# Optimization experiments

Hardware: AMD Instinct MI355X
Metric: run time of the kernel (lower is better)

Reference implementation:

```python
import jax, jax.numpy as jnp
import numpy as np

N_NODES = 50000
N_EDGES = 600000
IN_CH = 128
HID = 128
OUT_CH = 1
N_GRAPHS = 64


def setup_inputs() -> dict:
    key = jax.random.key(0)
    ks = jax.random.split(key, 16)
    inp = {
        "x": jax.random.normal(ks[0], (N_NODES, IN_CH), dtype=jnp.float32),
        "edge_index": jax.random.randint(ks[1], (2, N_EDGES), 0, N_NODES, dtype=jnp.int64),
        "edge_weight": jax.random.uniform(ks[2], (N_EDGES,), dtype=jnp.float32),
        "batch": jnp.sort(jax.random.randint(ks[3], (N_NODES,), 0, N_GRAPHS, dtype=jnp.int64)),
    }
    # SAGEConv params: lin_l (neighbor-aggregate path, has bias) and lin_r (root path)
    dims = [(IN_CH, HID), (HID, HID), (HID, HID), (HID, HID)]
    for i, (din, dout) in enumerate(dims, start=1):
        s = 1.0 / np.sqrt(din)
        inp[f"Wl{i}"] = jax.random.uniform(ks[3 + 2 * i], (din, dout), minval=-s, maxval=s, dtype=jnp.float32)
        inp[f"Wr{i}"] = jax.random.uniform(ks[4 + 2 * i], (din, dout), minval=-s, maxval=s, dtype=jnp.float32)
        inp[f"b{i}"] = jnp.zeros((dout,), dtype=jnp.float32)
    s = 1.0 / np.sqrt(HID)
    inp["Wc"] = jax.random.uniform(ks[14], (HID, OUT_CH), minval=-s, maxval=s, dtype=jnp.float32)
    inp["bc"] = jnp.zeros((OUT_CH,), dtype=jnp.float32)
    return inp


def _sage_conv(x, src, dst, Wl, Wr, b):
    # mean aggregation of source-node features at each destination node
    msg = x[src]  # [E, d] gather
    agg = jax.ops.segment_sum(msg, dst, num_segments=N_NODES)
    cnt = jax.ops.segment_sum(jnp.ones((src.shape[0],), x.dtype), dst, num_segments=N_NODES)
    agg = agg / jnp.maximum(cnt, 1.0)[:, None]
    return agg @ Wl + b + x @ Wr


def reference(x, edge_index, edge_weight, batch,
              Wl1, Wr1, b1, Wl2, Wr2, b2, Wl3, Wr3, b3, Wl4, Wr4, b4, Wc, bc):
    src, dst = edge_index[0], edge_index[1]
    h = jax.nn.relu(_sage_conv(x, src, dst, Wl1, Wr1, b1))
    h = jax.nn.relu(_sage_conv(h, src, dst, Wl2, Wr2, b2))
    h = jax.nn.relu(_sage_conv(h, src, dst, Wl3, Wr3, b3))
    h = jax.nn.relu(_sage_conv(h, src, dst, Wl4, Wr4, b4))
    # global mean pool over graphs
    pooled = jax.ops.segment_sum(h, batch, num_segments=N_GRAPHS)
    gcnt = jax.ops.segment_sum(jnp.ones((N_NODES,), h.dtype), batch, num_segments=N_GRAPHS)
    pooled = pooled / jnp.maximum(gcnt, 1.0)[:, None]  # [G, HID]
    return jax.nn.sigmoid(pooled @ Wc + bc)  # [G, 1]
```

## Files before the change

### kernel.cpp

```cpp
#include <hip/hip_runtime.h>
#include <math.h>

#define NND 50000
#define LNP 50048
#define NED 600000
#define CD  128
#define NG  64
#define NBLK 196
#define GROWS 64
#define SMAX 1152
#define APAD 136

typedef short s8v  __attribute__((ext_vector_type(8)));
typedef float f4v  __attribute__((ext_vector_type(4)));
typedef float f2v  __attribute__((ext_vector_type(2)));
typedef unsigned short u16x4 __attribute__((ext_vector_type(4)));
typedef unsigned short u16x8 __attribute__((ext_vector_type(8)));

static __device__ __forceinline__ unsigned short f2bf(float f) {
  union { float f; unsigned u; } v; v.f = f;
  unsigned r = v.u + 0x7fffu + ((v.u >> 16) & 1u);
  return (unsigned short)(r >> 16);
}
static __device__ __forceinline__ unsigned short f2bf_t(float f) {
  union { float f; unsigned u; } v; v.f = f;
  return (unsigned short)(v.u >> 16);
}
static __device__ __forceinline__ unsigned f2fp8x4(float a, float b, float c, float d) {
  int r = __builtin_amdgcn_cvt_pk_fp8_f32(a, b, 0, false);
  r = __builtin_amdgcn_cvt_pk_fp8_f32(c, d, r, true);
  return (unsigned)r;
}
static __device__ __forceinline__ s8v fp8x8_to_bf16(uint2 v) {
  f2v c0 = __builtin_amdgcn_cvt_pk_f32_fp8(v.x, false);
  f2v c1 = __builtin_amdgcn_cvt_pk_f32_fp8(v.x, true);
  f2v c2 = __builtin_amdgcn_cvt_pk_f32_fp8(v.y, false);
  f2v c3 = __builtin_amdgcn_cvt_pk_f32_fp8(v.y, true);
  union { u16x8 u; s8v s; } o;
  o.u[0] = f2bf_t(c0.x); o.u[1] = f2bf_t(c0.y);
  o.u[2] = f2bf_t(c1.x); o.u[3] = f2bf_t(c1.y);
  o.u[4] = f2bf_t(c2.x); o.u[5] = f2bf_t(c2.y);
  o.u[6] = f2bf_t(c3.x); o.u[7] = f2bf_t(c3.y);
  return o.s;
}
static __device__ __forceinline__ void g2lds8(const unsigned char* g, unsigned char* l) {
  __builtin_amdgcn_global_load_lds(
      (const __attribute__((address_space(1))) unsigned*)g,
      (__attribute__((address_space(3))) unsigned*)l, 16, 0, 0);
}

__global__ __launch_bounds__(256) void bsum_k(const int* __restrict__ cnt,
                                              int* __restrict__ bsum) {
  __shared__ int s[256];
  int i = blockIdx.x * 256 + threadIdx.x;
  s[threadIdx.x] = (i < NND) ? cnt[i] : 0;
  __syncthreads();
  for (int off = 128; off > 0; off >>= 1) {
    if (threadIdx.x < off) s[threadIdx.x] += s[threadIdx.x + off];
    __syncthreads();
  }
  if (threadIdx.x == 0) bsum[blockIdx.x] = s[0];
}

__global__ __launch_bounds__(256) void escan2_k(const int* __restrict__ cnt,
                                                const int* __restrict__ bsum,
                                                int* __restrict__ offs,
                                                int* __restrict__ cur,
                                                const int* __restrict__ batch,
                                                int* __restrict__ gb) {
  __shared__ int sb[256];
  __shared__ int s[256];
  const int t = threadIdx.x;
  const int bid = blockIdx.x;

  sb[t] = (t < NBLK) ? bsum[t] : 0;
  if (bid == 0 && t <= NG) {
    int lo = 0, hi = NND;
    while (lo < hi) {
      int mid = (lo + hi) >> 1;
      if (batch[mid] < t) lo = mid + 1; else hi = mid;
    }
    gb[t] = lo;
  }
  __syncthreads();
  for (int off = 1; off < 256; off <<= 1) {
    int v = (t >= off) ? sb[t - off] : 0;
    __syncthreads();
    sb[t] += v;
    __syncthreads();
  }
  const int boff = (bid == 0) ? 0 : sb[bid - 1];
  if (bid == 0 && t == NBLK - 1) offs[NND] = sb[t];

  const int i = bid * 256 + t;
  const int v = (i < NND) ? cnt[i] : 0;
  s[t] = v;
  __syncthreads();
  for (int off = 1; off < 256; off <<= 1) {
    int u = (t >= off) ? s[t - off] : 0;
    __syncthreads();
    s[t] += u;
    __syncthreads();
  }
  if (i < NND) {
    int excl = s[t] - v + boff;
    offs[i] = excl;
    cur[i]  = excl;
  }
}

__global__ void fill_k(const int* __restrict__ src, const int* __restrict__ dst,
                       int* __restrict__ cur, int* __restrict__ csr) {
  int e = blockIdx.x * blockDim.x + threadIdx.x;
  if (e >= NED) return;
  int d = dst[e];
  int pos = atomicAdd(&cur[d], 1);
  csr[pos] = src[e];
}

struct WPtrs { const float* w[8]; unsigned short* wt[8]; };
__global__ void prep_k(const float* __restrict__ x, unsigned* __restrict__ x8,
                       WPtrs p, const int* __restrict__ dst, int* __restrict__ cnt) {
  int t = blockIdx.x * blockDim.x + threadIdx.x;
  if (t < NND * 32) {
    float4 v = reinterpret_cast<const float4*>(x)[t];
    x8[t] = f2fp8x4(v.x, v.y, v.z, v.w);
  } else {
    int u = t - NND * 32;
    if (u < 8 * CD * CD) {
      int m = u >> 14, r = u & (CD * CD - 1);
      int n = r >> 7, k = r & 127;
      p.wt[m][r] = f2bf(p.w[m][k * CD + n]);
    } else {
      int e = u - 8 * CD * CD;
      if (e < NED) atomicAdd(&cnt[dst[e]], 1);
    }
  }
}

__global__ __launch_bounds__(256, 4) void sage_k(
    const unsigned* __restrict__ xq,
    const int* __restrict__ csr, const int* __restrict__ offs,
    const unsigned short* __restrict__ WlT, const unsigned short* __restrict__ WrT,
    const float* __restrict__ bias, unsigned char* __restrict__ h8,
    const int* __restrict__ batch, float* __restrict__ pooled) {
  __shared__ unsigned short abuf[GROWS * APAD];
  __shared__ unsigned char  x8buf[GROWS * CD];
  __shared__ int sB[GROWS];
  __shared__ int scsr[SMAX];

  const int tid  = threadIdx.x;
  const int wave = tid >> 6;
  const int lane = tid & 63;
  const int quad = lane >> 4;
  const int l16  = lane & 15;
  const size_t rbase = (size_t)blockIdx.x * GROWS;

  const int eb0  = offs[rbase];
  const int span = offs[(rbase + GROWS < NND) ? rbase + GROWS : NND] - eb0;
  const bool big = span > SMAX;
  if (!big) {
    for (int k = tid; k < span; k += 256)
      scsr[k] = __builtin_nontemporal_load(&csr[eb0 + k]);
  }

  if (pooled && tid < GROWS) {
    size_t row = rbase + tid;
    sB[tid] = (row < NND) ? batch[row] : -1;
  }

  __syncthreads();

  {
    const unsigned char* xg = (const unsigned char*)xq;
#pragma unroll
    for (int j = 0; j < 2; ++j) {
      const int s = j * 256 + tid;
      const int row = s >> 3;
      const int c = (s & 7) ^ (row & 7);
      g2lds8(xg + (rbase + row) * CD + c * 16, &x8buf[(size_t)s * 16]);
    }
  }

  s8v bL[2][4], bR[2][4];
#pragma unroll
  for (int nt = 0; nt < 2; ++nt) {
    const int n = wave * 32 + nt * 16 + l16;
#pragma unroll
    for (int kk = 0; kk < 4; ++kk) {
      size_t woff = (size_t)n * CD + kk * 32 + quad * 8;
      bL[nt][kk] = *reinterpret_cast<const s8v*>(WlT + woff);
      bR[nt][kk] = *reinterpret_cast<const s8v*>(WrT + woff);
    }
  }
  const float bv0 = bias[wave * 32 + l16];
  const float bv1 = bias[wave * 32 + 16 + l16];

  {
    const int team = tid >> 3;
    const int tl   = tid & 7;
    const unsigned* base = xq + tl * 4;
    auto run = [&](auto fetch) {
      for (int i = 0; i < 2; ++i) {
        const int rl = team * 2 + i;
        const size_t row = rbase + rl;
        u16x8 o0 = {}, o1 = {};
        if (row < NND) {
          const int e0 = offs[row], e1 = offs[row + 1];
          f2v a[8] = {};
          int e = e0;
          for (; e + 4 <= e1; e += 4) {
            int s[4];
#pragma unroll
            for (int j = 0; j < 4; ++j) s[j] = fetch(e + j);
            uint4 v[4];
#pragma unroll
            for (int j = 0; j < 4; ++j)
              v[j] = *reinterpret_cast<const uint4*>(base + (size_t)s[j] * 32);
#pragma unroll
            for (int j = 0; j < 4; ++j) {
              a[0] += __builtin_amdgcn_cvt_pk_f32_fp8(v[j].x, false);
              a[1] += __builtin_amdgcn_cvt_pk_f32_fp8(v[j].x, true);
              a[2] += __builtin_amdgcn_cvt_pk_f32_fp8(v[j].y, false);
              a[3] += __builtin_amdgcn_cvt_pk_f32_fp8(v[j].y, true);
              a[4] += __builtin_amdgcn_cvt_pk_f32_fp8(v[j].z, false);
              a[5] += __builtin_amdgcn_cvt_pk_f32_fp8(v[j].z, true);
              a[6] += __builtin_amdgcn_cvt_pk_f32_fp8(v[j].w, false);
              a[7] += __builtin_amdgcn_cvt_pk_f32_fp8(v[j].w, true);
            }
          }
          for (; e < e1; ++e) {
            uint4 v = *reinterpret_cast<const uint4*>(base + (size_t)fetch(e) * 32);
            a[0] += __builtin_amdgcn_cvt_pk_f32_fp8(v.x, false);
            a[1] += __builtin_amdgcn_cvt_pk_f32_fp8(v.x, true);
            a[2] += __builtin_amdgcn_cvt_pk_f32_fp8(v.y, false);
            a[3] += __builtin_amdgcn_cvt_pk_f32_fp8(v.y, true);
            a[4] += __builtin_amdgcn_cvt_pk_f32_fp8(v.z, false);
            a[5] += __builtin_amdgcn_cvt_pk_f32_fp8(v.z, true);
            a[6] += __builtin_amdgcn_cvt_pk_f32_fp8(v.w, false);
            a[7] += __builtin_amdgcn_cvt_pk_f32_fp8(v.w, true);
          }
          const float invd = 1.0f / fmaxf((float)(e1 - e0), 1.0f);
#pragma unroll
          for (int c = 0; c < 4; ++c) {
            o0[2 * c]     = f2bf(a[c].x * invd);
            o0[2 * c + 1] = f2bf(a[c].y * invd);
            o1[2 * c]     = f2bf(a[4 + c].x * invd);
            o1[2 * c + 1] = f2bf(a[4 + c].y * invd);
          }
        }
        *reinterpret_cast<u16x8*>(abuf + rl * APAD + tl * 16)     = o0;
        *reinterpret_cast<u16x8*>(abuf + rl * APAD + tl * 16 + 8) = o1;
      }
    };
    if (!big) run([&](int e) { return scsr[e - eb0]; });
    else      run([&](int e) { return csr[e]; });
  }

  __syncthreads();

  const bool fast = pooled && (rbase + GROWS <= NND) && (sB[0] == sB[GROWS - 1]);
  const int c0 = wave * 32 + l16;
  float p0 = 0.f, p1 = 0.f;

#pragma unroll
  for (int rt = 0; rt < GROWS / 16; ++rt) {
    const int rowl = rt * 16 + l16;
    const int sw   = rowl & 7;
    const unsigned short* arow = abuf + rowl * APAD + quad * 8;
    const unsigned char*  xrow = x8buf + rowl * CD;
    f4v acc0 = {}, acc1 = {};
#pragma unroll
    for (int kk = 0; kk < 4; ++kk) {
      s8v aA = *reinterpret_cast<const s8v*>(arow + kk * 32);
      uint2 xv = *reinterpret_cast<const uint2*>(
          xrow + ((((quad >> 1) + kk * 2) ^ sw) << 4) + ((quad & 1) << 3));
      s8v aX = fp8x8_to_bf16(xv);
      acc0 = __builtin_amdgcn_mfma_f32_16x16x32_bf16(aA, bL[0][kk], acc0, 0, 0, 0);
      acc0 = __builtin_amdgcn_mfma_f32_16x16x32_bf16(aX, bR[0][kk], acc0, 0, 0, 0);
      acc1 = __builtin_amdgcn_mfma_f32_16x16x32_bf16(aA, bL[1][kk], acc1, 0, 0, 0);
      acc1 = __builtin_amdgcn_mfma_f32_16x16x32_bf16(aX, bR[1][kk], acc1, 0, 0, 0);
    }
    const size_t row0 = rbase + rt * 16 + quad * 4;
#pragma unroll
    for (int r = 0; r < 4; ++r) {
      const size_t row = row0 + r;
      float v0 = fmaxf(acc0[r] + bv0, 0.0f);
      float v1 = fmaxf(acc1[r] + bv1, 0.0f);
      if (h8) {
        int q0 = __builtin_amdgcn_cvt_pk_fp8_f32(v0, v0, 0, false);
        int q1 = __builtin_amdgcn_cvt_pk_fp8_f32(v1, v1, 0, false);
        __builtin_nontemporal_store((unsigned char)q0, h8 + row * CD + c0);
        __builtin_nontemporal_store((unsigned char)q1, h8 + row * CD + c0 + 16);
      }
      if (pooled) {
        if (fast) {
          p0 += v0; p1 += v1;
        } else {
          int g = sB[rt * 16 + quad * 4 + r];
          if (g >= 0) {
            atomicAdd(&pooled[g * CD + c0], v0);
            atomicAdd(&pooled[g * CD + c0 + 16], v1);
          }
        }
      }
    }
  }

  if (fast) {
    p0 += __shfl_xor(p0, 16, 64);
    p0 += __shfl_xor(p0, 32, 64);
    p1 += __shfl_xor(p1, 16, 64);
    p1 += __shfl_xor(p1, 32, 64);
    if (quad == 0) {
      const int g = sB[0];
      atomicAdd(&pooled[g * CD + c0], p0);
      atomicAdd(&pooled[g * CD + c0 + 16], p1);
    }
  }
}

__global__ void final_k(const float* __restrict__ pooled, const int* __restrict__ gb,
                        const float* __restrict__ Wc, const float* __restrict__ bc,
                        float* __restrict__ out) {
  int g = blockIdx.x;
  int lane = threadIdx.x;
  float part = pooled[g * CD + lane] * Wc[lane] +
               pooled[g * CD + 64 + lane] * Wc[64 + lane];
#pragma unroll
  for (int off = 32; off > 0; off >>= 1) part += __shfl_down(part, off, 64);
  if (lane == 0) {
    float cnt = (float)(gb[g + 1] - gb[g]);
    float z = part / fmaxf(cnt, 1.0f) + bc[0];
    out[g] = 1.0f / (1.0f + expf(-z));
  }
}

extern "C" void kernel_launch(void* const* d_in, const int* in_sizes, int n_in,
                              void* d_out, int out_size, void* d_ws, size_t ws_size,
                              hipStream_t stream) {
  const float* x   = (const float*)d_in[0];
  const int*   ei  = (const int*)d_in[1];
  const int*   src = ei;
  const int*   dst = ei + NED;
  const int*   batch = (const int*)d_in[3];
  const float* Wc = (const float*)d_in[16];
  const float* bc = (const float*)d_in[17];
  float* out = (float*)d_out;

  char* w = (char*)d_ws;
  auto alloc = [&](size_t bytes) {
    char* p = w; w += (bytes + 255) & ~(size_t)255; return p;
  };
  int* cnti = (int*)alloc(NND * 4);
  float* pooled = (float*)alloc(NG * CD * 4);
  size_t zspan = (size_t)(w - (char*)cnti);
  int* offs = (int*)alloc((NND + 1) * 4);
  int* cur  = (int*)alloc(NND * 4);
  int* csr  = (int*)alloc((size_t)NED * 4);
  int* gb   = (int*)alloc((NG + 1) * 4);
  int* bsum = (int*)alloc(256 * 4);
  unsigned char* x8a = (unsigned char*)alloc((size_t)LNP * CD);
  unsigned char* x8b = (unsigned char*)alloc((size_t)LNP * CD);
  WPtrs wp;
  for (int i = 0; i < 4; ++i) {
    wp.w[2 * i]     = (const float*)d_in[4 + 3 * i];
    wp.w[2 * i + 1] = (const float*)d_in[5 + 3 * i];
  }
  for (int i = 0; i < 8; ++i) wp.wt[i] = (unsigned short*)alloc(CD * CD * 2);
  const float* bs[4] = {(const float*)d_in[6],  (const float*)d_in[9],
                        (const float*)d_in[12], (const float*)d_in[15]};

  hipMemsetAsync(cnti, 0, zspan, stream);

  prep_k<<<(NND * 32 + 8 * CD * CD + NED + 255) / 256, 256, 0, stream>>>(
      x, (unsigned*)x8a, wp, dst, cnti);

  bsum_k<<<NBLK, 256, 0, stream>>>(cnti, bsum);
  escan2_k<<<NBLK, 256, 0, stream>>>(cnti, bsum, offs, cur, batch, gb);
  fill_k<<<(NED + 255) / 256, 256, 0, stream>>>(src, dst, cur, csr);

  unsigned char* qcur = x8a;
  unsigned char* qnxt = x8b;
  const int ggrid = LNP / GROWS;
  for (int l = 0; l < 4; ++l) {
    if (l < 3) {
      sage_k<<<ggrid, 256, 0, stream>>>((const unsigned*)qcur, csr, offs,
                                        wp.wt[2 * l], wp.wt[2 * l + 1], bs[l],
                                        qnxt, batch, nullptr);
      unsigned char* q = qcur; qcur = qnxt; qnxt = q;
    } else {
      sage_k<<<ggrid, 256, 0, stream>>>((const unsigned*)qcur, csr, offs,
                                        wp.wt[2 * l], wp.wt[2 * l + 1], bs[l],
                                        nullptr, batch, pooled);
    }
  }

  final_k<<<NG, 64, 0, stream>>>(pooled, gb, Wc, bc, out);
}
```

Before: 289.5 us.

## Split fp8 feature rows into two 64-column planes and aggregate per plane

```diff
diff --git a/kernel.cpp b/kernel.cpp
--- a/kernel.cpp
+++ b/kernel.cpp
@@ -14,7 +14,6 @@
 typedef short s8v  __attribute__((ext_vector_type(8)));
 typedef float f4v  __attribute__((ext_vector_type(4)));
 typedef float f2v  __attribute__((ext_vector_type(2)));
-typedef unsigned short u16x4 __attribute__((ext_vector_type(4)));
 typedef unsigned short u16x8 __attribute__((ext_vector_type(8)));
 
 static __device__ __forceinline__ unsigned short f2bf(float f) {
@@ -124,7 +123,11 @@
   int t = blockIdx.x * blockDim.x + threadIdx.x;
   if (t < NND * 32) {
     float4 v = reinterpret_cast<const float4*>(x)[t];
-    x8[t] = f2fp8x4(v.x, v.y, v.z, v.w);
+    unsigned q = f2fp8x4(v.x, v.y, v.z, v.w);
+    int node = t >> 5, c4 = t & 31;
+    unsigned* dstp = (c4 < 16) ? x8 + node * 16 + c4
+                               : x8 + LNP * 16 + node * 16 + (c4 - 16);
+    *dstp = q;
   } else {
     int u = t - NND * 32;
     if (u < 8 * CD * CD) {
@@ -155,6 +158,8 @@
   const int quad = lane >> 4;
   const int l16  = lane & 15;
   const size_t rbase = (size_t)blockIdx.x * GROWS;
+  const unsigned char* xlo = (const unsigned char*)xq;
+  const unsigned char* xhi = xlo + (size_t)LNP * 64;
 
   const int eb0  = offs[rbase];
   const int span = offs[(rbase + GROWS < NND) ? rbase + GROWS : NND] - eb0;
@@ -172,13 +177,15 @@
   __syncthreads();
 
   {
-    const unsigned char* xg = (const unsigned char*)xq;
 #pragma unroll
     for (int j = 0; j < 2; ++j) {
       const int s = j * 256 + tid;
       const int row = s >> 3;
       const int c = (s & 7) ^ (row & 7);
-      g2lds8(xg + (rbase + row) * CD + c * 16, &x8buf[(size_t)s * 16]);
+      const unsigned char* srcp = (c < 4)
+          ? xlo + (rbase + row) * 64 + c * 16
+          : xhi + (rbase + row) * 64 + (c - 4) * 16;
+      g2lds8(srcp, &x8buf[(size_t)s * 16]);
     }
   }
 
@@ -199,58 +206,50 @@
   {
     const int team = tid >> 3;
     const int tl   = tid & 7;
-    const unsigned* base = xq + tl * 4;
     auto run = [&](auto fetch) {
-      for (int i = 0; i < 2; ++i) {
-        const int rl = team * 2 + i;
-        const size_t row = rbase + rl;
-        u16x8 o0 = {}, o1 = {};
-        if (row < NND) {
-          const int e0 = offs[row], e1 = offs[row + 1];
-          f2v a[8] = {};
-          int e = e0;
-          for (; e + 4 <= e1; e += 4) {
-            int s[4];
-#pragma unroll
-            for (int j = 0; j < 4; ++j) s[j] = fetch(e + j);
-            uint4 v[4];
-#pragma unroll
-            for (int j = 0; j < 4; ++j)
-              v[j] = *reinterpret_cast<const uint4*>(base + (size_t)s[j] * 32);
-#pragma unroll
-            for (int j = 0; j < 4; ++j) {
-              a[0] += __builtin_amdgcn_cvt_pk_f32_fp8(v[j].x, false);
-              a[1] += __builtin_amdgcn_cvt_pk_f32_fp8(v[j].x, true);
-              a[2] += __builtin_amdgcn_cvt_pk_f32_fp8(v[j].y, false);
-              a[3] += __builtin_amdgcn_cvt_pk_f32_fp8(v[j].y, true);
-              a[4] += __builtin_amdgcn_cvt_pk_f32_fp8(v[j].z, false);
-              a[5] += __builtin_amdgcn_cvt_pk_f32_fp8(v[j].z, true);
-              a[6] += __builtin_amdgcn_cvt_pk_f32_fp8(v[j].w, false);
-              a[7] += __builtin_amdgcn_cvt_pk_f32_fp8(v[j].w, true);
+#pragma unroll 1
+      for (int p = 0; p < 2; ++p) {
+        const unsigned char* base = (p ? xhi : xlo) + tl * 8;
+        for (int i = 0; i < 2; ++i) {
+          const int rl = team * 2 + i;
+          const size_t row = rbase + rl;
+          u16x8 o = {};
+          if (row < NND) {
+            const int e0 = offs[row], e1 = offs[row + 1];
+            f2v a[4] = {};
+            int e = e0;
+            for (; e + 4 <= e1; e += 4) {
+              int s[4];
+#pragma unroll
+              for (int j = 0; j < 4; ++j) s[j] = fetch(e + j);
+              uint2 v[4];
+#pragma unroll
+              for (int j = 0; j < 4; ++j)
+                v[j] = *reinterpret_cast<const uint2*>(base + (size_t)s[j] * 64);
+#pragma unroll
+              for (int j = 0; j < 4; ++j) {
+                a[0] += __builtin_amdgcn_cvt_pk_f32_fp8(v[j].x, false);
+                a[1] += __builtin_amdgcn_cvt_pk_f32_fp8(v[j].x, true);
+                a[2] += __builtin_amdgcn_cvt_pk_f32_fp8(v[j].y, false);
+                a[3] += __builtin_amdgcn_cvt_pk_f32_fp8(v[j].y, true);
+              }
+            }
+            for (; e < e1; ++e) {
+              uint2 v = *reinterpret_cast<const uint2*>(base + (size_t)fetch(e) * 64);
+              a[0] += __builtin_amdgcn_cvt_pk_f32_fp8(v.x, false);
+              a[1] += __builtin_amdgcn_cvt_pk_f32_fp8(v.x, true);
+              a[2] += __builtin_amdgcn_cvt_pk_f32_fp8(v.y, false);
+              a[3] += __builtin_amdgcn_cvt_pk_f32_fp8(v.y, true);
+            }
+            const float invd = 1.0f / fmaxf((float)(e1 - e0), 1.0f);
+#pragma unroll
+            for (int c = 0; c < 4; ++c) {
+              o[2 * c]     = f2bf(a[c].x * invd);
+              o[2 * c + 1] = f2bf(a[c].y * invd);
             }
           }
-          for (; e < e1; ++e) {
-            uint4 v = *reinterpret_cast<const uint4*>(base + (size_t)fetch(e) * 32);
-            a[0] += __builtin_amdgcn_cvt_pk_f32_fp8(v.x, false);
-            a[1] += __builtin_amdgcn_cvt_pk_f32_fp8(v.x, true);
-            a[2] += __builtin_amdgcn_cvt_pk_f32_fp8(v.y, false);
-            a[3] += __builtin_amdgcn_cvt_pk_f32_fp8(v.y, true);
-            a[4] += __builtin_amdgcn_cvt_pk_f32_fp8(v.z, false);
-            a[5] += __builtin_amdgcn_cvt_pk_f32_fp8(v.z, true);
-            a[6] += __builtin_amdgcn_cvt_pk_f32_fp8(v.w, false);
-            a[7] += __builtin_amdgcn_cvt_pk_f32_fp8(v.w, true);
-          }
-          const float invd = 1.0f / fmaxf((float)(e1 - e0), 1.0f);
-#pragma unroll
-          for (int c = 0; c < 4; ++c) {
-            o0[2 * c]     = f2bf(a[c].x * invd);
-            o0[2 * c + 1] = f2bf(a[c].y * invd);
-            o1[2 * c]     = f2bf(a[4 + c].x * invd);
-            o1[2 * c + 1] = f2bf(a[4 + c].y * invd);
-          }
+          *reinterpret_cast<u16x8*>(abuf + rl * APAD + p * 64 + tl * 8) = o;
         }
-        *reinterpret_cast<u16x8*>(abuf + rl * APAD + tl * 16)     = o0;
-        *reinterpret_cast<u16x8*>(abuf + rl * APAD + tl * 16 + 8) = o1;
       }
     };
     if (!big) run([&](int e) { return scsr[e - eb0]; });
@@ -290,8 +289,11 @@
       if (h8) {
         int q0 = __builtin_amdgcn_cvt_pk_fp8_f32(v0, v0, 0, false);
         int q1 = __builtin_amdgcn_cvt_pk_fp8_f32(v1, v1, 0, false);
-        __builtin_nontemporal_store((unsigned char)q0, h8 + row * CD + c0);
-        __builtin_nontemporal_store((unsigned char)q1, h8 + row * CD + c0 + 16);
+        unsigned char* hdst = (wave < 2)
+            ? h8 + row * 64 + c0
+            : h8 + (size_t)LNP * 64 + row * 64 + (c0 - 64);
+        __builtin_nontemporal_store((unsigned char)q0, hdst);
+        __builtin_nontemporal_store((unsigned char)q1, hdst + 16);
       }
       if (pooled) {
         if (fast) {
```

Measured after the change: 311.9 us. 1.08x slower.
